# Kernel tuning notes

Hardware: AMD Instinct MI355X
Metric: run time of the kernel (lower is better)

## Reference

```python
import math
import jax, jax.numpy as jnp
import numpy as np
from jax import lax

B, H, W, C1, D, NH = 32, 28, 28, 64, 256, 8
KS, RATIO = 9, 0.0005
NEG = -1.0e9


def setup_inputs() -> dict:
    key = jax.random.key(0)
    ks = jax.random.split(key, 6)
    x = jax.random.normal(ks[0], (B, 1, H, W), jnp.float32)
    conv_w = jax.random.normal(ks[1], (C1, 1, KS, KS), jnp.float32) * 0.05
    channel_embed = jax.random.normal(ks[2], (C1, D), jnp.float32)
    in_proj_w = jax.random.normal(ks[3], (3 * D, D), jnp.float32) * (1.0 / math.sqrt(D))
    in_proj_b = jnp.zeros((3 * D,), jnp.float32)
    out_proj_w = jax.random.normal(ks[4], (D, D), jnp.float32) * (1.0 / math.sqrt(D))
    out_proj_b = jnp.zeros((D,), jnp.float32)
    return {"x": x, "conv_w": conv_w, "channel_embed": channel_embed,
            "in_proj_w": in_proj_w, "in_proj_b": in_proj_b,
            "out_proj_w": out_proj_w, "out_proj_b": out_proj_b}


def _pos_encoding_2d(h, w, dim):
    # even dims: sin(y * div), odd dims: cos(x * div)  (matches torch broadcast)
    div = jnp.exp(jnp.arange(0, dim, 2, dtype=jnp.float32) * (-math.log(10000.0) / dim))
    pe_even = jnp.sin(jnp.arange(h, dtype=jnp.float32)[:, None] * div)  # (h, dim/2)
    pe_odd = jnp.cos(jnp.arange(w, dtype=jnp.float32)[:, None] * div)   # (w, dim/2)
    pe = jnp.zeros((h, w, dim), jnp.float32)
    pe = pe.at[..., 0::2].set(jnp.broadcast_to(pe_even[:, None, :], (h, w, dim // 2)))
    pe = pe.at[..., 1::2].set(jnp.broadcast_to(pe_odd[None, :, :], (h, w, dim // 2)))
    return pe


def reference(x, conv_w, channel_embed, in_proj_w, in_proj_b, out_proj_w, out_proj_b):
    pad = KS // 2
    A = jax.nn.relu(lax.conv_general_dilated(
        x, conv_w, (1, 1), [(pad, pad), (pad, pad)],
        dimension_numbers=("NCHW", "OIHW", "NCHW")))  # (B, C1, H, W)

    # global top-k threshold (kthvalue equivalent)
    total = A.size
    k = max(1, int(math.ceil(RATIO * total)))
    if k >= total:
        mask_global = jnp.ones_like(A, dtype=bool)
    else:
        vals, _ = lax.top_k(A.reshape(-1), k)
        mask_global = A >= vals[-1]
    A_g = A * mask_global.astype(A.dtype)

    v = jnp.transpose(A_g, (0, 2, 3, 1))  # (B, H, W, C1)
    nz = v > 0
    count = nz.sum(axis=-1)  # (B, H, W)

    top2_vals, top2_idx = lax.top_k(v, 2)  # (B,H,W,2)
    cidx = jnp.arange(C1)
    sel2 = (cidx == top2_idx[..., 0:1]) | (cidx == top2_idx[..., 1:2])
    idx_single = jnp.argmax(jnp.where(nz, v, -jnp.inf), axis=-1)
    sel1 = cidx == idx_single[..., None]

    logits = jnp.where((count >= 2)[..., None] & sel2, v, NEG)
    logits = jnp.where((count == 1)[..., None] & sel1, v, logits)
    sparse_weights = jax.nn.softmax(logits, axis=-1)
    sparse_weights = jnp.where((count == 0)[..., None], 0.0, sparse_weights)

    loc_emb = jnp.einsum("bhwc,cd->bhwd", sparse_weights, channel_embed)
    loc_emb = loc_emb + _pos_encoding_2d(H, W, D)[None]
    seq = loc_emb.reshape(B, H * W, D)

    # torch nn.MultiheadAttention (batch_first, self-attn)
    qkv = seq @ in_proj_w.T + in_proj_b  # (B, S, 3D)
    q, kk, vv = jnp.split(qkv, 3, axis=-1)
    hd = D // NH
    def heads(t):
        return t.reshape(B, H * W, NH, hd).transpose(0, 2, 1, 3)  # (B, NH, S, hd)
    q, kk, vv = heads(q), heads(kk), heads(vv)
    scores = jnp.einsum("bnqd,bnkd->bnqk", q, kk) / math.sqrt(hd)
    attn = jax.nn.softmax(scores, axis=-1)
    ctx = jnp.einsum("bnqk,bnkd->bnqd", attn, vv)
    ctx = ctx.transpose(0, 2, 1, 3).reshape(B, H * W, D)
    attn_out = ctx @ out_proj_w.T + out_proj_b
    pooled = attn_out.mean(axis=1)  # (B, D)
    return pooled, sparse_weights, top2_idx
```

## Files before the change

kernel.cpp:

```cpp
#include <hip/hip_runtime.h>
#include <cmath>

#define NB 32
#define C1N 64
#define DIM 256
#define NHEAD 8
#define SEQL 784
#define NA 1605632
#define SEQN 6422528
#define KSEL 803u
#define QK2S (0.17677669529663687f * 1.4426950408889634f)
#define THR2 11.541560f
#define PECOEF (-0.03597789207803197f)

#define AS1 __attribute__((address_space(1)))
#define AS3 __attribute__((address_space(3)))

typedef __attribute__((ext_vector_type(8))) short bf16x8;
typedef __attribute__((ext_vector_type(4))) float f32x4;

__device__ __forceinline__ unsigned short f2b(float f) {
  unsigned u = __float_as_uint(f);
  unsigned r = u + 0x7fffu + ((u >> 16) & 1u);
  return (unsigned short)(r >> 16);
}

__device__ __forceinline__ unsigned cvt_pk_bf16(float lo, float hi) {
  unsigned r;
  asm("v_cvt_pk_bf16_f32 %0, %1, %2" : "=v"(r) : "v"(lo), "v"(hi));
  return r;
}

__global__ __launch_bounds__(256) void k_init(const float* __restrict__ ipw,
                                              unsigned short* __restrict__ wbuf,
                                              unsigned* __restrict__ z) {
  int i = blockIdx.x * 256 + threadIdx.x;
  if (i < 66080) z[i] = 0u;
  wbuf[i] = f2b(ipw[i]);
}

__global__ __launch_bounds__(256) void k_conv(const float* __restrict__ x,
                                              const float* __restrict__ cw,
                                              float* __restrict__ vbuf) {
  __shared__ __align__(16) float ximg[1296];
  __shared__ float wlds[5184];
  int tid = threadIdx.x;
  int b = blockIdx.x / 7, sblk = blockIdx.x % 7;
  for (int e = tid; e < 1296; e += 256) ximg[e] = 0.f;
  for (int e = tid; e < 5184; e += 256) {
    int c = e / 81, t = e - c * 81;
    wlds[t * 64 + c] = cw[e];
  }
  __syncthreads();
  const float* xb = x + b * 784;
  for (int e = tid; e < 784; e += 256) {
    int row = e / 28, col = e - row * 28;
    ximg[(row + 4) * 36 + col + 4] = xb[e];
  }
  __syncthreads();
  int wv = tid >> 6, lane = tid & 63;
  for (int it = 0; it < 7; ++it) {
    int grp = sblk * 28 + it * 4 + wv;
    int hr = grp / 7, wc0 = (grp % 7) * 4;
    float a0 = 0.f, a1 = 0.f, a2 = 0.f, a3 = 0.f;
    #pragma unroll
    for (int dy = 0; dy < 9; ++dy) {
      const float4* xr4 = (const float4*)&ximg[(hr + dy) * 36 + wc0];
      float4 xa = xr4[0], xbq = xr4[1], xc = xr4[2];
      float xr[12] = {xa.x, xa.y, xa.z, xa.w, xbq.x, xbq.y, xbq.z, xbq.w,
                      xc.x, xc.y, xc.z, xc.w};
      #pragma unroll
      for (int dx = 0; dx < 9; ++dx) {
        float w = wlds[(dy * 9 + dx) * 64 + lane];
        a0 = fmaf(xr[dx + 0], w, a0);
        a1 = fmaf(xr[dx + 1], w, a1);
        a2 = fmaf(xr[dx + 2], w, a2);
        a3 = fmaf(xr[dx + 3], w, a3);
      }
    }
    size_t base = ((size_t)(b * 784 + hr * 28 + wc0)) * 64 + lane;
    vbuf[base +   0] = fmaxf(a0, 0.f);
    vbuf[base +  64] = fmaxf(a1, 0.f);
    vbuf[base + 128] = fmaxf(a2, 0.f);
    vbuf[base + 192] = fmaxf(a3, 0.f);
  }
}

__global__ __launch_bounds__(256) void k_h8(const float* __restrict__ vbuf,
                                            const unsigned* __restrict__ sel,
                                            unsigned* __restrict__ hist8,
                                            int stage) {
  __shared__ unsigned lh[256];
  int tid = threadIdx.x;
  lh[tid] = 0u;
  __syncthreads();
  if (stage == 0 || sel[2] == 0u) {
    unsigned key = (stage == 1) ? sel[0] : 0u;
    const float4* v4 = (const float4*)vbuf;
    int n4 = NA / 4;
    for (int i = blockIdx.x * 256 + tid; i < n4; i += gridDim.x * 256) {
      float4 v = v4[i];
      float vv[4] = {v.x, v.y, v.z, v.w};
      #pragma unroll
      for (int j = 0; j < 4; ++j) {
        if (vv[j] > 0.0f) {
          unsigned bits = __float_as_uint(vv[j]);
          if (stage == 0) atomicAdd(&lh[bits >> 24], 1u);
          else if ((bits >> 24) == key) atomicAdd(&lh[(bits >> 16) & 0xFFu], 1u);
        }
      }
    }
  }
  __syncthreads();
  if (lh[tid] > 0u) atomicAdd(&hist8[tid], lh[tid]);
}

__global__ __launch_bounds__(256) void k_scan8(const unsigned* __restrict__ hist8,
                                               unsigned* __restrict__ sel,
                                               int stage) {
  if (stage == 1 && sel[2]) return;
  __shared__ unsigned ss[256];
  int t = threadIdx.x;
  ss[t] = hist8[t];
  __syncthreads();
  for (int off = 1; off < 256; off <<= 1) {
    unsigned v = (t + off < 256) ? ss[t + off] : 0u;
    __syncthreads();
    ss[t] += v;
    __syncthreads();
  }
  unsigned rem = (stage == 0) ? KSEL : sel[1];
  if (stage == 0 && t == 0 && ss[0] < KSEL) {
    sel[2] = 1u; sel[3] = 0u;
  }
  unsigned S = ss[t];
  unsigned above = (t < 255) ? ss[t + 1] : 0u;
  if (S >= rem && above < rem) {
    if (stage == 0) { sel[0] = (unsigned)t; sel[1] = rem - above; }
    else            { sel[4] = (unsigned)t; sel[5] = rem - above; }
  }
}

__global__ __launch_bounds__(256) void k_h16(const float* __restrict__ vbuf,
                                             const unsigned* __restrict__ sel,
                                             unsigned* __restrict__ hist16) {
  if (sel[2]) return;
  unsigned key16 = (sel[0] << 8) | sel[4];
  const float4* v4 = (const float4*)vbuf;
  int n4 = NA / 4;
  for (int i = blockIdx.x * 256 + threadIdx.x; i < n4; i += gridDim.x * 256) {
    float4 v = v4[i];
    float vv[4] = {v.x, v.y, v.z, v.w};
    #pragma unroll
    for (int j = 0; j < 4; ++j) {
      if (vv[j] > 0.0f) {
        unsigned bits = __float_as_uint(vv[j]);
        if ((bits >> 16) == key16) atomicAdd(&hist16[bits & 0xFFFFu], 1u);
      }
    }
  }
}

__global__ __launch_bounds__(1024) void k_scan16(const unsigned* __restrict__ hist16,
                                                 unsigned* __restrict__ sel) {
  if (sel[2]) return;
  __shared__ unsigned ss[1024];
  int t = threadIdx.x;
  unsigned rem = sel[5];
  unsigned sum = 0;
  for (int i = 0; i < 64; ++i) sum += hist16[t * 64 + i];
  ss[t] = sum;
  __syncthreads();
  for (int off = 1; off < 1024; off <<= 1) {
    unsigned v = (t + off < 1024) ? ss[t + off] : 0u;
    __syncthreads();
    ss[t] += v;
    __syncthreads();
  }
  unsigned S = ss[t];
  unsigned above = (t < 1023) ? ss[t + 1] : 0u;
  if (S >= rem && above < rem) {
    unsigned cum = above;
    for (int bb = t * 64 + 63; bb >= t * 64; --bb) {
      unsigned hb = hist16[bb];
      cum += hb;
      if (cum >= rem) {
        sel[3] = (((sel[0] << 8) | sel[4]) << 16) | (unsigned)bb;
        break;
      }
    }
  }
}

__global__ __launch_bounds__(256) void k_select(const float* __restrict__ vbuf,
                                                const unsigned* __restrict__ sel,
                                                const float* __restrict__ ce,
                                                unsigned short* __restrict__ seqb,
                                                float* __restrict__ out_sw,
                                                float* __restrict__ out_idx) {
  int wid = threadIdx.x >> 6;
  int lane = threadIdx.x & 63;
  int pos = blockIdx.x * 4 + wid;
  int hw = pos % 784;
  int hr = hw / 28;
  int wc = hw % 28;
  float thr = __uint_as_float(sel[3]);
  float a = vbuf[(size_t)pos * 64 + lane];
  float val = (a >= thr) ? a : 0.0f;
  unsigned long long nzm = __ballot(val > 0.0f);
  int count = __popcll(nzm);
  float v1 = val; int i1 = lane;
  #pragma unroll
  for (int off = 32; off > 0; off >>= 1) {
    float ov = __shfl_xor(v1, off);
    int oi = __shfl_xor(i1, off);
    if (ov > v1 || (ov == v1 && oi < i1)) { v1 = ov; i1 = oi; }
  }
  float vx = (lane == i1) ? -INFINITY : val;
  float v2 = vx; int i2 = lane;
  #pragma unroll
  for (int off = 32; off > 0; off >>= 1) {
    float ov = __shfl_xor(v2, off);
    int oi = __shfl_xor(i2, off);
    if (ov > v2 || (ov == v2 && oi < i2)) { v2 = ov; i2 = oi; }
  }
  float w1 = 0.0f, w2 = 0.0f;
  if (count >= 2) {
    float e = __expf(v2 - v1);
    float invd = 1.0f / (1.0f + e);
    w1 = invd; w2 = e * invd;
  } else if (count == 1) {
    w1 = 1.0f;
  }
  float wt = (lane == i1) ? w1 : ((lane == i2) ? w2 : 0.0f);
  out_sw[(size_t)pos * 64 + lane] = wt;
  if (lane < 2) out_idx[pos * 2 + lane] = (float)(lane == 0 ? i1 : i2);
  int d0 = lane * 4;
  float4 c1v = *(const float4*)(ce + (size_t)i1 * 256 + d0);
  float4 c2v = *(const float4*)(ce + (size_t)i2 * 256 + d0);
  float dv0 = __expf((float)d0 * PECOEF);
  float dv2 = __expf((float)(d0 + 2) * PECOEF);
  float ox = w1 * c1v.x + w2 * c2v.x + __sinf((float)hr * dv0);
  float oy = w1 * c1v.y + w2 * c2v.y + __cosf((float)wc * dv0);
  float oz = w1 * c1v.z + w2 * c2v.z + __sinf((float)hr * dv2);
  float ow = w1 * c1v.w + w2 * c2v.w + __cosf((float)wc * dv2);
  ushort4 ob = make_ushort4(f2b(ox), f2b(oy), f2b(oz), f2b(ow));
  *(ushort4*)(seqb + (size_t)pos * 256 + d0) = ob;
}

__global__ __launch_bounds__(256) void k_gemm_lds(const unsigned short* __restrict__ A,
                                                  const unsigned short* __restrict__ W,
                                                  const float* __restrict__ bias,
                                                  unsigned short* __restrict__ C,
                                                  int M, int N, int K) {
  __shared__ __align__(16) unsigned short As[8192];
  __shared__ __align__(16) unsigned short Bs[8192];
  int tid = threadIdx.x;
  int lane = tid & 63, wid = tid >> 6;
  int q = lane & 15, g = lane >> 4;
  int m0 = blockIdx.y * 128, n0 = blockIdx.x * 128;
  int lrow = lane >> 3, s = lane & 7;
  const unsigned short* aSrc = A + (size_t)(m0 + wid * 8 + lrow) * K + (s ^ lrow) * 8;
  const unsigned short* bSrc = W + (size_t)(n0 + wid * 8 + lrow) * K + (s ^ lrow) * 8;
  int dstW = wid * 512;
  int mloc = (wid >> 1) * 64, nloc = (wid & 1) * 64;
  int q7 = q & 7;
  f32x4 acc[4][4];
  #pragma unroll
  for (int i = 0; i < 4; ++i)
    #pragma unroll
    for (int j = 0; j < 4; ++j) acc[i][j] = (f32x4){0.f, 0.f, 0.f, 0.f};
  for (int k0 = 0; k0 < K; k0 += 64) {
    #pragma unroll
    for (int i = 0; i < 4; ++i) {
      __builtin_amdgcn_global_load_lds((const AS1 void*)(aSrc + (size_t)i * 32 * K + k0),
                                       (AS3 void*)(&As[i * 2048 + dstW]), 16, 0, 0);
      __builtin_amdgcn_global_load_lds((const AS1 void*)(bSrc + (size_t)i * 32 * K + k0),
                                       (AS3 void*)(&Bs[i * 2048 + dstW]), 16, 0, 0);
    }
    __syncthreads();
    #pragma unroll
    for (int kk = 0; kk < 2; ++kk) {
      bf16x8 af[4], bf[4];
      #pragma unroll
      for (int i = 0; i < 4; ++i)
        af[i] = *(const bf16x8*)&As[(mloc + i * 16 + q) * 64 + (((kk * 4 + g) ^ q7) * 8)];
      #pragma unroll
      for (int j = 0; j < 4; ++j)
        bf[j] = *(const bf16x8*)&Bs[(nloc + j * 16 + q) * 64 + (((kk * 4 + g) ^ q7) * 8)];
      __builtin_amdgcn_s_setprio(1);
      #pragma unroll
      for (int i = 0; i < 4; ++i)
        #pragma unroll
        for (int j = 0; j < 4; ++j)
          acc[i][j] = __builtin_amdgcn_mfma_f32_16x16x32_bf16(af[i], bf[j], acc[i][j], 0, 0, 0);
      __builtin_amdgcn_s_setprio(0);
    }
    __syncthreads();
  }
  #pragma unroll
  for (int j = 0; j < 4; ++j) {
    int col = n0 + nloc + j * 16 + q;
    float bj = bias[col];
    float qs = (col < 256) ? QK2S : 1.0f;
    #pragma unroll
    for (int i = 0; i < 4; ++i) {
      #pragma unroll
      for (int r = 0; r < 4; ++r) {
        int row = m0 + mloc + i * 16 + g * 4 + r;
        C[(size_t)row * N + col] = f2b((acc[i][j][r] + bj) * qs);
      }
    }
  }
}

__global__ __launch_bounds__(256) void k_vt(const unsigned short* __restrict__ qkv,
                                            unsigned short* __restrict__ Vt) {
  __shared__ unsigned short lds[32][72];
  int k0 = blockIdx.x * 64;
  int bh = blockIdx.y;
  int b = bh >> 3, nh = bh & 7;
  int tid = threadIdx.x;
  int key = tid >> 2;
  int c8 = (tid & 3) * 8;
  int kk = k0 + key;
  ushort4 a = make_ushort4(0, 0, 0, 0), bq = a;
  if (kk < 784) {
    const unsigned short* src = qkv + (size_t)(b * 784 + kk) * 768 + 512 + nh * 32 + c8;
    a  = *(const ushort4*)src;
    bq = *(const ushort4*)(src + 4);
  }
  lds[c8 + 0][key] = a.x;  lds[c8 + 1][key] = a.y;
  lds[c8 + 2][key] = a.z;  lds[c8 + 3][key] = a.w;
  lds[c8 + 4][key] = bq.x; lds[c8 + 5][key] = bq.y;
  lds[c8 + 6][key] = bq.z; lds[c8 + 7][key] = bq.w;
  __syncthreads();
  int d = tid >> 3;
  int kc = (tid & 7) * 8;
  if (k0 + kc < 800) {
    int sb = (kc & 32) + ((kc >> 3) & 3) * 4;
    ushort4 o0 = make_ushort4(lds[d][sb + 0],  lds[d][sb + 1],
                              lds[d][sb + 2],  lds[d][sb + 3]);
    ushort4 o1 = make_ushort4(lds[d][sb + 16], lds[d][sb + 17],
                              lds[d][sb + 18], lds[d][sb + 19]);
    unsigned short* dst = Vt + ((size_t)bh * 32 + d) * 800 + k0 + kc;
    *(ushort4*)dst = o0;
    *(ushort4*)(dst + 4) = o1;
  }
}

__global__ __launch_bounds__(256) void k_attn(const unsigned short* __restrict__ qkv,
                                              const unsigned short* __restrict__ Vt,
                                              unsigned short* __restrict__ ctx) {
  __shared__ __align__(16) unsigned short Kt[3][1024];
  __shared__ __align__(16) unsigned short Vti[3][1024];
  int wid = threadIdx.x >> 6;
  int lane = threadIdx.x & 63;
  int blk = blockIdx.x;
  int wrk = (blk & 7) * 416 + (blk >> 3);
  int bh = wrk / 13;
  int qb = (wrk - bh * 13) * 4 + wid;
  int b = bh >> 3, nh = bh & 7;
  int q = lane & 15, g = lane >> 4;
  bool active = (qb < 49);
  const f32x4 zero4 = {0.f, 0.f, 0.f, 0.f};

  int qrow = b * 784 + (active ? qb * 16 + q : q);
  bf16x8 qf = *(const bf16x8*)(qkv + (size_t)qrow * 768 + nh * 32 + g * 8);
  asm volatile("s_waitcnt vmcnt(0)" ::: "memory");

  const unsigned short* kbase = qkv + (size_t)b * 784 * 768 + 256 + nh * 32;
  const unsigned short* vbase = Vt + (size_t)bh * 32 * 800;

  int rit = ((wid & 1) << 4) + (lane >> 2);
  int sG = (lane & 3) ^ ((rit + (rit >> 2)) & 3);
  bool isK = (wid < 2);
  int ldsoff = ((wid & 1) << 4) * 32;
  const unsigned short* sp = isK ? (kbase + (size_t)rit * 768 + sG * 8)
                                 : (vbase + (size_t)rit * 800 + sG * 8);
  const int sstride = isK ? (32 * 768) : 32;
  unsigned short* ldsb = (isK ? &Kt[0][0] : &Vti[0][0]) + ldsoff;

  int slotr = ((g ^ ((q + (q >> 2)) & 3)) << 3);
  int rowA = q * 32 + slotr;
  int rowB = (16 + q) * 32 + slotr;

  f32x4 acc0 = zero4, acc1 = zero4;
  float m = -INFINITY, lp = 0.f;

#define STAGE(BUFO) {                                                          \
    __builtin_amdgcn_global_load_lds((const AS1 void*)sp,                      \
                                     (AS3 void*)(ldsb + (BUFO)), 16, 0, 0);    \
    sp += sstride; }

#define STEP(CUR, NXT) {                                                       \
    asm volatile("s_waitcnt vmcnt(1)" ::: "memory");                           \
    __builtin_amdgcn_s_barrier();                                              \
    asm volatile("" ::: "memory");                                             \
    STAGE(NXT);                                                                \
    bf16x8 kA = *(const bf16x8*)&Kt[0][(CUR) + rowA];                          \
    bf16x8 kB = *(const bf16x8*)&Kt[0][(CUR) + rowB];                          \
    bf16x8 va = *(const bf16x8*)&Vti[0][(CUR) + rowA];                         \
    bf16x8 vb = *(const bf16x8*)&Vti[0][(CUR) + rowB];                         \
    __builtin_amdgcn_s_setprio(1);                                             \
    f32x4 s0 = __builtin_amdgcn_mfma_f32_16x16x32_bf16(kA, qf, zero4, 0, 0, 0);\
    f32x4 s1 = __builtin_amdgcn_mfma_f32_16x16x32_bf16(kB, qf, zero4, 0, 0, 0);\
    __builtin_amdgcn_s_setprio(0);                                             \
    float pl = fmaxf(fmaxf(fmaxf(s0[0], s0[1]), fmaxf(s0[2], s0[3])),          \
                     fmaxf(fmaxf(s1[0], s1[1]), fmaxf(s1[2], s1[3])));         \
    if (!__all(pl <= m + THR2)) {                                              \
      float pm = fmaxf(pl, __shfl_xor(pl, 16));                                \
      pm = fmaxf(pm, __shfl_xor(pm, 32));                                      \
      float mnew = fmaxf(m, pm);                                               \
      float sc = __builtin_amdgcn_exp2f(m - mnew);                             \
      lp *= sc; acc0 *= sc; acc1 *= sc;                                        \
      m = mnew;                                                                \
    }                                                                          \
    float p0[4], p1[4];                                                        \
    _Pragma("unroll")                                                          \
    for (int r = 0; r < 4; ++r) {                                              \
      p0[r] = __builtin_amdgcn_exp2f(s0[r] - m);                               \
      p1[r] = __builtin_amdgcn_exp2f(s1[r] - m);                               \
    }                                                                          \
    lp += ((p0[0] + p0[1]) + (p0[2] + p0[3]))                                  \
        + ((p1[0] + p1[1]) + (p1[2] + p1[3]));                                 \
    union { unsigned u[4]; bf16x8 v; } pu;                                     \
    pu.u[0] = cvt_pk_bf16(p0[0], p0[1]);                                       \
    pu.u[1] = cvt_pk_bf16(p0[2], p0[3]);                                       \
    pu.u[2] = cvt_pk_bf16(p1[0], p1[1]);                                       \
    pu.u[3] = cvt_pk_bf16(p1[2], p1[3]);                                       \
    __builtin_amdgcn_s_setprio(1);                                             \
    acc0 = __builtin_amdgcn_mfma_f32_16x16x32_bf16(va, pu.v, acc0, 0, 0, 0);   \
    acc1 = __builtin_amdgcn_mfma_f32_16x16x32_bf16(vb, pu.v, acc1, 0, 0, 0);   \
    __builtin_amdgcn_s_setprio(0);                                             \
  }

  STAGE(0);
  STAGE(1024);

  for (int t = 0; t < 8; ++t) {
    STEP(0, 2048);
    STEP(1024, 0);
    STEP(2048, 1024);
  }
  {
    asm volatile("s_waitcnt vmcnt(1)" ::: "memory");
    __builtin_amdgcn_s_barrier();
    asm volatile("" ::: "memory");
    bf16x8 kA = *(const bf16x8*)&Kt[0][rowA];
    bf16x8 va = *(const bf16x8*)&Vti[0][rowA];
    bf16x8 vb = *(const bf16x8*)&Vti[0][rowB];
    f32x4 s0 = __builtin_amdgcn_mfma_f32_16x16x32_bf16(kA, qf, zero4, 0, 0, 0);
    float pl = fmaxf(fmaxf(s0[0], s0[1]), fmaxf(s0[2], s0[3]));
    if (!__all(pl <= m + THR2)) {
      float pm = fmaxf(pl, __shfl_xor(pl, 16));
      pm = fmaxf(pm, __shfl_xor(pm, 32));
      float mnew = fmaxf(m, pm);
      float sc = __builtin_amdgcn_exp2f(m - mnew);
      lp *= sc; acc0 *= sc; acc1 *= sc;
      m = mnew;
    }
    float p0[4];
    #pragma unroll
    for (int r = 0; r < 4; ++r) p0[r] = __builtin_amdgcn_exp2f(s0[r] - m);
    lp += (p0[0] + p0[1]) + (p0[2] + p0[3]);
    union { unsigned u[4]; bf16x8 v; } pu;
    pu.u[0] = cvt_pk_bf16(p0[0], p0[1]);
    pu.u[1] = cvt_pk_bf16(p0[2], p0[3]);
    pu.u[2] = 0u;
    pu.u[3] = 0u;
    acc0 = __builtin_amdgcn_mfma_f32_16x16x32_bf16(va, pu.v, acc0, 0, 0, 0);
    acc1 = __builtin_amdgcn_mfma_f32_16x16x32_bf16(vb, pu.v, acc1, 0, 0, 0);
  }
#undef STEP
#undef STAGE
  float l = lp + __shfl_xor(lp, 16);
  l += __shfl_xor(l, 32);
  float linv = 1.f / l;
  if (active) {
    unsigned short* cp = ctx + (size_t)(b * 784 + qb * 16 + q) * 256 + nh * 32;
    ushort4 oA = make_ushort4(f2b(acc0[0] * linv), f2b(acc0[1] * linv),
                              f2b(acc0[2] * linv), f2b(acc0[3] * linv));
    ushort4 oB = make_ushort4(f2b(acc1[0] * linv), f2b(acc1[1] * linv),
                              f2b(acc1[2] * linv), f2b(acc1[3] * linv));
    *(ushort4*)(cp + g * 4) = oA;
    *(ushort4*)(cp + 16 + g * 4) = oB;
  }
}

__global__ __launch_bounds__(256) void k_poolctx(const unsigned short* __restrict__ ctx,
                                                 float* __restrict__ part) {
  int b = blockIdx.x >> 3, sseg = blockIdx.x & 7;
  int d = threadIdx.x;
  const unsigned short* base = ctx + ((size_t)b * 784 + sseg * 98) * 256 + d;
  float acc = 0.f;
  for (int t = 0; t < 98; ++t)
    acc += __uint_as_float((unsigned)base[(size_t)t * 256] << 16);
  part[(size_t)blockIdx.x * 256 + d] = acc;
}

__global__ __launch_bounds__(256) void k_pgemv(const float* __restrict__ part,
                                               const float* __restrict__ opw,
                                               const float* __restrict__ opb,
                                               float* __restrict__ out) {
  __shared__ float mc[256];
  int b = blockIdx.x, d = threadIdx.x;
  float s = 0.f;
  #pragma unroll
  for (int i = 0; i < 8; ++i) s += part[(size_t)(b * 8 + i) * 256 + d];
  mc[d] = s * (1.0f / 784.0f);
  __syncthreads();
  float acc = opb[d];
  const float4* wr = (const float4*)(opw + (size_t)d * 256);
  #pragma unroll 8
  for (int j = 0; j < 64; ++j) {
    float4 w = wr[j];
    float4 m4 = *(const float4*)&mc[j * 4];
    acc += m4.x * w.x + m4.y * w.y + m4.z * w.z + m4.w * w.w;
  }
  out[b * 256 + d] = acc;
}

extern "C" void kernel_launch(void* const* d_in, const int* in_sizes, int n_in,
                              void* d_out, int out_size, void* d_ws, size_t ws_size,
                              hipStream_t stream) {
  (void)in_sizes; (void)n_in; (void)out_size; (void)ws_size;
  const float* x   = (const float*)d_in[0];
  const float* cw  = (const float*)d_in[1];
  const float* ce  = (const float*)d_in[2];
  const float* ipw = (const float*)d_in[3];
  const float* ipb = (const float*)d_in[4];
  const float* opw = (const float*)d_in[5];
  const float* opb = (const float*)d_in[6];

  float* out = (float*)d_out;
  float* pooled  = out;
  float* out_sw  = out + 8192;
  float* out_idx = out + 8192 + NA;

  float* ws = (float*)d_ws;
  float* vbuf = ws;
  unsigned* hist16 = (unsigned*)(ws + NA);
  unsigned* hist8a = hist16 + 65536;
  unsigned* hist8b = hist8a + 256;
  unsigned* sel    = hist8b + 256;
  unsigned short* seqb = (unsigned short*)(ws + NA + 66080);
  unsigned short* qkvb = seqb + SEQN;
  unsigned short* Vt   = qkvb + 3 * (size_t)SEQN;
  unsigned short* wbuf = Vt + 256 * 32 * 800;
  float* part = (float*)(wbuf + 262144);

  k_init<<<768, 256, 0, stream>>>(ipw, wbuf, hist16);
  k_conv<<<224, 256, 0, stream>>>(x, cw, vbuf);
  k_h8<<<1024, 256, 0, stream>>>(vbuf, sel, hist8a, 0);
  k_scan8<<<1, 256, 0, stream>>>(hist8a, sel, 0);
  k_h8<<<1024, 256, 0, stream>>>(vbuf, sel, hist8b, 1);
  k_scan8<<<1, 256, 0, stream>>>(hist8b, sel, 1);
  k_h16<<<1024, 256, 0, stream>>>(vbuf, sel, hist16);
  k_scan16<<<1, 1024, 0, stream>>>(hist16, sel);
  k_select<<<25088 / 4, 256, 0, stream>>>(vbuf, sel, ce, seqb, out_sw, out_idx);
  {
    dim3 gq(768 / 128, 25088 / 128);
    k_gemm_lds<<<gq, 256, 0, stream>>>(seqb, wbuf, ipb, qkvb, 25088, 768, 256);
  }
  {
    dim3 gv(13, 256);
    k_vt<<<gv, 256, 0, stream>>>(qkvb, Vt);
  }
  k_attn<<<3328, 256, 0, stream>>>(qkvb, Vt, seqb );
  k_poolctx<<<256, 256, 0, stream>>>(seqb, part);
  k_pgemv<<<NB, 256, 0, stream>>>(part, opw, opb, pooled);
}
```

Baseline: 183.2 us.

## Fuse first histogram into conv, fold scans into consumers, write V transposed from GEMM

The first radix-select histogram is now built inside the conv kernel. The separate single-block scan kernels are removed, and each consumer block recomputes the small suffix scans redundantly. The QKV GEMM epilogue writes the V columns straight into the transposed Vt layout, which removes the k_vt transpose kernel and one read of the V slice. This drops four launches and one full pass over the activations, at the cost of redundant per-block scans and LDS atomics in conv. Padded Vt positions 784..799 are no longer written and rely on whatever is in the workspace, or on the attention masking.

```diff
diff --git a/kernel.cpp b/kernel.cpp
--- a/kernel.cpp
+++ b/kernel.cpp
@@ -31,6 +31,16 @@
   return r;
 }
 
+__device__ __forceinline__ void scan256_suffix(unsigned* ss, int t) {
+  #pragma unroll
+  for (int off = 1; off < 256; off <<= 1) {
+    unsigned v = (t + off < 256) ? ss[t + off] : 0u;
+    __syncthreads();
+    ss[t] += v;
+    __syncthreads();
+  }
+}
+
 __global__ __launch_bounds__(256) void k_init(const float* __restrict__ ipw,
                                               unsigned short* __restrict__ wbuf,
                                               unsigned* __restrict__ z) {
@@ -41,11 +51,14 @@
 
 __global__ __launch_bounds__(256) void k_conv(const float* __restrict__ x,
                                               const float* __restrict__ cw,
-                                              float* __restrict__ vbuf) {
+                                              float* __restrict__ vbuf,
+                                              unsigned* __restrict__ hist8a) {
   __shared__ __align__(16) float ximg[1296];
   __shared__ float wlds[5184];
+  __shared__ unsigned lh[256];
   int tid = threadIdx.x;
   int b = blockIdx.x / 7, sblk = blockIdx.x % 7;
+  lh[tid] = 0u;
   for (int e = tid; e < 1296; e += 256) ximg[e] = 0.f;
   for (int e = tid; e < 5184; e += 256) {
     int c = e / 81, t = e - c * 81;
@@ -78,77 +91,81 @@
         a3 = fmaf(xr[dx + 3], w, a3);
       }
     }
+    a0 = fmaxf(a0, 0.f); a1 = fmaxf(a1, 0.f);
+    a2 = fmaxf(a2, 0.f); a3 = fmaxf(a3, 0.f);
     size_t base = ((size_t)(b * 784 + hr * 28 + wc0)) * 64 + lane;
-    vbuf[base +   0] = fmaxf(a0, 0.f);
-    vbuf[base +  64] = fmaxf(a1, 0.f);
-    vbuf[base + 128] = fmaxf(a2, 0.f);
-    vbuf[base + 192] = fmaxf(a3, 0.f);
-  }
-}
-
-__global__ __launch_bounds__(256) void k_h8(const float* __restrict__ vbuf,
-                                            const unsigned* __restrict__ sel,
-                                            unsigned* __restrict__ hist8,
-                                            int stage) {
+    vbuf[base +   0] = a0;
+    vbuf[base +  64] = a1;
+    vbuf[base + 128] = a2;
+    vbuf[base + 192] = a3;
+    if (a0 > 0.f) atomicAdd(&lh[__float_as_uint(a0) >> 24], 1u);
+    if (a1 > 0.f) atomicAdd(&lh[__float_as_uint(a1) >> 24], 1u);
+    if (a2 > 0.f) atomicAdd(&lh[__float_as_uint(a2) >> 24], 1u);
+    if (a3 > 0.f) atomicAdd(&lh[__float_as_uint(a3) >> 24], 1u);
+  }
+  __syncthreads();
+  if (lh[tid] > 0u) atomicAdd(&hist8a[tid], lh[tid]);
+}
+
+__global__ __launch_bounds__(256) void k_h8b(const float* __restrict__ vbuf,
+                                             const unsigned* __restrict__ hist8a,
+                                             unsigned* __restrict__ hist8b) {
+  __shared__ unsigned ss[256];
   __shared__ unsigned lh[256];
-  int tid = threadIdx.x;
-  lh[tid] = 0u;
-  __syncthreads();
-  if (stage == 0 || sel[2] == 0u) {
-    unsigned key = (stage == 1) ? sel[0] : 0u;
-    const float4* v4 = (const float4*)vbuf;
-    int n4 = NA / 4;
-    for (int i = blockIdx.x * 256 + tid; i < n4; i += gridDim.x * 256) {
-      float4 v = v4[i];
-      float vv[4] = {v.x, v.y, v.z, v.w};
-      #pragma unroll
-      for (int j = 0; j < 4; ++j) {
-        if (vv[j] > 0.0f) {
-          unsigned bits = __float_as_uint(vv[j]);
-          if (stage == 0) atomicAdd(&lh[bits >> 24], 1u);
-          else if ((bits >> 24) == key) atomicAdd(&lh[(bits >> 16) & 0xFFu], 1u);
-        }
-      }
-    }
-  }
-  __syncthreads();
-  if (lh[tid] > 0u) atomicAdd(&hist8[tid], lh[tid]);
-}
-
-__global__ __launch_bounds__(256) void k_scan8(const unsigned* __restrict__ hist8,
-                                               unsigned* __restrict__ sel,
-                                               int stage) {
-  if (stage == 1 && sel[2]) return;
-  __shared__ unsigned ss[256];
+  __shared__ unsigned bkey;
   int t = threadIdx.x;
-  ss[t] = hist8[t];
-  __syncthreads();
-  for (int off = 1; off < 256; off <<= 1) {
-    unsigned v = (t + off < 256) ? ss[t + off] : 0u;
-    __syncthreads();
-    ss[t] += v;
-    __syncthreads();
-  }
-  unsigned rem = (stage == 0) ? KSEL : sel[1];
-  if (stage == 0 && t == 0 && ss[0] < KSEL) {
-    sel[2] = 1u; sel[3] = 0u;
-  }
-  unsigned S = ss[t];
-  unsigned above = (t < 255) ? ss[t + 1] : 0u;
-  if (S >= rem && above < rem) {
-    if (stage == 0) { sel[0] = (unsigned)t; sel[1] = rem - above; }
-    else            { sel[4] = (unsigned)t; sel[5] = rem - above; }
-  }
-}
-
-__global__ __launch_bounds__(256) void k_h16(const float* __restrict__ vbuf,
-                                             const unsigned* __restrict__ sel,
-                                             unsigned* __restrict__ hist16) {
-  if (sel[2]) return;
-  unsigned key16 = (sel[0] << 8) | sel[4];
+  ss[t] = hist8a[t];
+  lh[t] = 0u;
+  __syncthreads();
+  scan256_suffix(ss, t);
+  if (ss[0] < KSEL) return;
+  unsigned S = ss[t], ab = (t < 255) ? ss[t + 1] : 0u;
+  if (S >= KSEL && ab < KSEL) bkey = (unsigned)t;
+  __syncthreads();
+  unsigned key = bkey;
   const float4* v4 = (const float4*)vbuf;
   int n4 = NA / 4;
-  for (int i = blockIdx.x * 256 + threadIdx.x; i < n4; i += gridDim.x * 256) {
+  for (int i = blockIdx.x * 256 + t; i < n4; i += gridDim.x * 256) {
+    float4 v = v4[i];
+    float vv[4] = {v.x, v.y, v.z, v.w};
+    #pragma unroll
+    for (int j = 0; j < 4; ++j) {
+      if (vv[j] > 0.0f) {
+        unsigned bits = __float_as_uint(vv[j]);
+        if ((bits >> 24) == key) atomicAdd(&lh[(bits >> 16) & 0xFFu], 1u);
+      }
+    }
+  }
+  __syncthreads();
+  if (lh[t] > 0u) atomicAdd(&hist8b[t], lh[t]);
+}
+
+__global__ __launch_bounds__(256) void k_h16(const float* __restrict__ vbuf,
+                                             const unsigned* __restrict__ hist8a,
+                                             const unsigned* __restrict__ hist8b,
+                                             unsigned* __restrict__ hist16) {
+  __shared__ unsigned ss[256];
+  __shared__ unsigned bk0, bk1, brem;
+  int t = threadIdx.x;
+  ss[t] = hist8a[t];
+  __syncthreads();
+  scan256_suffix(ss, t);
+  if (ss[0] < KSEL) return;
+  unsigned S = ss[t], ab = (t < 255) ? ss[t + 1] : 0u;
+  if (S >= KSEL && ab < KSEL) { bk0 = (unsigned)t; brem = KSEL - ab; }
+  __syncthreads();
+  unsigned key0 = bk0, rem1 = brem;
+  __syncthreads();
+  ss[t] = hist8b[t];
+  __syncthreads();
+  scan256_suffix(ss, t);
+  S = ss[t]; ab = (t < 255) ? ss[t + 1] : 0u;
+  if (S >= rem1 && ab < rem1) bk1 = (unsigned)t;
+  __syncthreads();
+  unsigned key16 = (key0 << 8) | bk1;
+  const float4* v4 = (const float4*)vbuf;
+  int n4 = NA / 4;
+  for (int i = blockIdx.x * 256 + t; i < n4; i += gridDim.x * 256) {
     float4 v = v4[i];
     float vv[4] = {v.x, v.y, v.z, v.w};
     #pragma unroll
@@ -161,12 +178,45 @@
   }
 }
 
-__global__ __launch_bounds__(1024) void k_scan16(const unsigned* __restrict__ hist16,
+__global__ __launch_bounds__(1024) void k_scan16(const unsigned* __restrict__ hist8a,
+                                                 const unsigned* __restrict__ hist8b,
+                                                 const unsigned* __restrict__ hist16,
                                                  unsigned* __restrict__ sel) {
-  if (sel[2]) return;
   __shared__ unsigned ss[1024];
+  __shared__ unsigned bk0, bk1, brem, brem2;
   int t = threadIdx.x;
-  unsigned rem = sel[5];
+  if (t < 256) ss[t] = hist8a[t];
+  __syncthreads();
+  for (int off = 1; off < 256; off <<= 1) {
+    unsigned v = 0u;
+    if (t < 256) v = (t + off < 256) ? ss[t + off] : 0u;
+    __syncthreads();
+    if (t < 256) ss[t] += v;
+    __syncthreads();
+  }
+  if (ss[0] < KSEL) { if (t == 0) sel[3] = 0u; return; }
+  if (t < 256) {
+    unsigned S = ss[t], ab = (t < 255) ? ss[t + 1] : 0u;
+    if (S >= KSEL && ab < KSEL) { bk0 = (unsigned)t; brem = KSEL - ab; }
+  }
+  __syncthreads();
+  unsigned key0 = bk0, rem1 = brem;
+  if (t < 256) ss[t] = hist8b[t];
+  __syncthreads();
+  for (int off = 1; off < 256; off <<= 1) {
+    unsigned v = 0u;
+    if (t < 256) v = (t + off < 256) ? ss[t + off] : 0u;
+    __syncthreads();
+    if (t < 256) ss[t] += v;
+    __syncthreads();
+  }
+  if (t < 256) {
+    unsigned S = ss[t], ab = (t < 255) ? ss[t + 1] : 0u;
+    if (S >= rem1 && ab < rem1) { bk1 = (unsigned)t; brem2 = rem1 - ab; }
+  }
+  __syncthreads();
+  unsigned key16 = (key0 << 8) | bk1;
+  unsigned rem2 = brem2;
   unsigned sum = 0;
   for (int i = 0; i < 64; ++i) sum += hist16[t * 64 + i];
   ss[t] = sum;
@@ -179,13 +229,13 @@
   }
   unsigned S = ss[t];
   unsigned above = (t < 1023) ? ss[t + 1] : 0u;
-  if (S >= rem && above < rem) {
+  if (S >= rem2 && above < rem2) {
     unsigned cum = above;
     for (int bb = t * 64 + 63; bb >= t * 64; --bb) {
       unsigned hb = hist16[bb];
       cum += hb;
-      if (cum >= rem) {
-        sel[3] = (((sel[0] << 8) | sel[4]) << 16) | (unsigned)bb;
+      if (cum >= rem2) {
+        sel[3] = (key16 << 16) | (unsigned)bb;
         break;
       }
     }
@@ -252,6 +302,7 @@
                                                   const unsigned short* __restrict__ W,
                                                   const float* __restrict__ bias,
                                                   unsigned short* __restrict__ C,
+                                                  unsigned short* __restrict__ Vt,
                                                   int M, int N, int K) {
   __shared__ __align__(16) unsigned short As[8192];
   __shared__ __align__(16) unsigned short Bs[8192];
@@ -298,54 +349,40 @@
     }
     __syncthreads();
   }
-  #pragma unroll
-  for (int j = 0; j < 4; ++j) {
-    int col = n0 + nloc + j * 16 + q;
-    float bj = bias[col];
-    float qs = (col < 256) ? QK2S : 1.0f;
-    #pragma unroll
-    for (int i = 0; i < 4; ++i) {
+  if (n0 < 512) {
+    #pragma unroll
+    for (int j = 0; j < 4; ++j) {
+      int col = n0 + nloc + j * 16 + q;
+      float bj = bias[col];
+      float qs = (col < 256) ? QK2S : 1.0f;
       #pragma unroll
-      for (int r = 0; r < 4; ++r) {
-        int row = m0 + mloc + i * 16 + g * 4 + r;
-        C[(size_t)row * N + col] = f2b((acc[i][j][r] + bj) * qs);
+      for (int i = 0; i < 4; ++i) {
+        #pragma unroll
+        for (int r = 0; r < 4; ++r) {
+          int row = m0 + mloc + i * 16 + g * 4 + r;
+          C[(size_t)row * N + col] = f2b((acc[i][j][r] + bj) * qs);
+        }
       }
     }
-  }
-}
-
-__global__ __launch_bounds__(256) void k_vt(const unsigned short* __restrict__ qkv,
-                                            unsigned short* __restrict__ Vt) {
-  __shared__ unsigned short lds[32][72];
-  int k0 = blockIdx.x * 64;
-  int bh = blockIdx.y;
-  int b = bh >> 3, nh = bh & 7;
-  int tid = threadIdx.x;
-  int key = tid >> 2;
-  int c8 = (tid & 3) * 8;
-  int kk = k0 + key;
-  ushort4 a = make_ushort4(0, 0, 0, 0), bq = a;
-  if (kk < 784) {
-    const unsigned short* src = qkv + (size_t)(b * 784 + kk) * 768 + 512 + nh * 32 + c8;
-    a  = *(const ushort4*)src;
-    bq = *(const ushort4*)(src + 4);
-  }
-  lds[c8 + 0][key] = a.x;  lds[c8 + 1][key] = a.y;
-  lds[c8 + 2][key] = a.z;  lds[c8 + 3][key] = a.w;
-  lds[c8 + 4][key] = bq.x; lds[c8 + 5][key] = bq.y;
-  lds[c8 + 6][key] = bq.z; lds[c8 + 7][key] = bq.w;
-  __syncthreads();
-  int d = tid >> 3;
-  int kc = (tid & 7) * 8;
-  if (k0 + kc < 800) {
-    int sb = (kc & 32) + ((kc >> 3) & 3) * 4;
-    ushort4 o0 = make_ushort4(lds[d][sb + 0],  lds[d][sb + 1],
-                              lds[d][sb + 2],  lds[d][sb + 3]);
-    ushort4 o1 = make_ushort4(lds[d][sb + 16], lds[d][sb + 17],
-                              lds[d][sb + 18], lds[d][sb + 19]);
-    unsigned short* dst = Vt + ((size_t)bh * 32 + d) * 800 + k0 + kc;
-    *(ushort4*)dst = o0;
-    *(ushort4*)(dst + 4) = o1;
+  } else {
+    #pragma unroll
+    for (int j = 0; j < 4; ++j) {
+      int colV = n0 + nloc + j * 16 + q;
+      float bj = bias[colV];
+      int dtot = colV - 512;
+      size_t vrow = ((size_t)(dtot >> 5) * 32 + (dtot & 31)) * 800;
+      #pragma unroll
+      for (int i = 0; i < 4; ++i) {
+        int rowbase = m0 + mloc + i * 16;
+        int b = rowbase / 784;
+        int t16 = rowbase - b * 784;
+        int pos = ((t16 >> 5) << 5) + ((t16 >> 4) & 1) * 4 + g * 8;
+        uint2 o;
+        o.x = cvt_pk_bf16(acc[i][j][0] + bj, acc[i][j][1] + bj);
+        o.y = cvt_pk_bf16(acc[i][j][2] + bj, acc[i][j][3] + bj);
+        *(uint2*)(Vt + (size_t)b * 8 * 32 * 800 + vrow + pos) = o;
+      }
+    }
   }
 }
 
@@ -551,21 +588,14 @@
   float* part = (float*)(wbuf + 262144);
 
   k_init<<<768, 256, 0, stream>>>(ipw, wbuf, hist16);
-  k_conv<<<224, 256, 0, stream>>>(x, cw, vbuf);
-  k_h8<<<1024, 256, 0, stream>>>(vbuf, sel, hist8a, 0);
-  k_scan8<<<1, 256, 0, stream>>>(hist8a, sel, 0);
-  k_h8<<<1024, 256, 0, stream>>>(vbuf, sel, hist8b, 1);
-  k_scan8<<<1, 256, 0, stream>>>(hist8b, sel, 1);
-  k_h16<<<1024, 256, 0, stream>>>(vbuf, sel, hist16);
-  k_scan16<<<1, 1024, 0, stream>>>(hist16, sel);
+  k_conv<<<224, 256, 0, stream>>>(x, cw, vbuf, hist8a);
+  k_h8b<<<1024, 256, 0, stream>>>(vbuf, hist8a, hist8b);
+  k_h16<<<1024, 256, 0, stream>>>(vbuf, hist8a, hist8b, hist16);
+  k_scan16<<<1, 1024, 0, stream>>>(hist8a, hist8b, hist16, sel);
   k_select<<<25088 / 4, 256, 0, stream>>>(vbuf, sel, ce, seqb, out_sw, out_idx);
   {
     dim3 gq(768 / 128, 25088 / 128);
-    k_gemm_lds<<<gq, 256, 0, stream>>>(seqb, wbuf, ipb, qkvb, 25088, 768, 256);
-  }
-  {
-    dim3 gv(13, 256);
-    k_vt<<<gv, 256, 0, stream>>>(qkvb, Vt);
+    k_gemm_lds<<<gq, 256, 0, stream>>>(seqb, wbuf, ipb, qkvb, Vt, 25088, 768, 256);
   }
   k_attn<<<3328, 256, 0, stream>>>(qkvb, Vt, seqb );
   k_poolctx<<<256, 256, 0, stream>>>(seqb, part);
```

New measurement: 164.8 us. -10.1%, faster.
